# Optimization experiments

Hardware: AMD Instinct MI355X
Metric: run time of the kernel (lower is better)

The kernel has to match this reference:

```python
import jax, jax.numpy as jnp
import numpy as np

SEQ_LEN = 4096
D_IN = 2048
D_OUT = 2048
DROPOUT_P = 0.5


def setup_inputs() -> dict:
    key = jax.random.key(0)
    kx, kq, kk, kv = jax.random.split(key, 4)
    return {
        "x": jax.random.normal(kx, (SEQ_LEN, D_IN), dtype=jnp.float32),
        "W_query": jax.random.uniform(kq, (D_IN, D_OUT), dtype=jnp.float32),
        "W_key": jax.random.uniform(kk, (D_IN, D_OUT), dtype=jnp.float32),
        "W_value": jax.random.uniform(kv, (D_IN, D_OUT), dtype=jnp.float32),
    }


def reference(x, W_query, W_key, W_value):
    # projections: [S, d_in] @ [d_in, d_out] -> [S, d_out]
    queries = x @ W_query
    keys = x @ W_key
    values = x @ W_value
    # full score matrix [S, S]
    attn_scores = queries @ keys.T
    S = attn_scores.shape[0]
    causal_mask = jnp.triu(jnp.ones((S, S), dtype=bool), k=1)
    masked = jnp.where(causal_mask, -jnp.inf, attn_scores)
    scale = jnp.sqrt(jnp.asarray(keys.shape[-1], dtype=masked.dtype))
    attn_weights = jax.nn.softmax(masked / scale, axis=1)
    # dropout p=0.5 (train mode), inverted scaling, deterministic key
    keep = jax.random.bernoulli(jax.random.key(42), 1.0 - DROPOUT_P, attn_weights.shape)
    attn_weights = jnp.where(keep, attn_weights / (1.0 - DROPOUT_P), 0.0)
    context_vec = attn_weights @ values  # [S, d_out]
    return context_vec
```

## Files before the change

### kernel.cpp

```cpp
#include <hip/hip_runtime.h>
#include <cstdint>
#include <cstddef>
#include <cmath>

#define SEQ 4096
#define DM  2048

typedef unsigned int u32;
typedef unsigned short u16;
typedef __attribute__((ext_vector_type(8))) short bf16x8;
typedef __attribute__((ext_vector_type(4))) float f32x4;
typedef __attribute__((ext_vector_type(16))) float f32x16;

__device__ __forceinline__ u16 f2bf(float f) {
  u32 u = __float_as_uint(f);
  return (u16)((u + 0x7FFFu + ((u >> 16) & 1u)) >> 16);
}
__device__ __forceinline__ float bf2f(u16 h) { return __uint_as_float(((u32)h) << 16); }

__device__ __forceinline__ size_t s_base(int row) {
  const int b = row >> 7;
  return (size_t)8192 * b * (b + 1) + (size_t)128 * (row & 127) * (b + 1);
}

__device__ __forceinline__ u32 rotl32(u32 x, int r) { return (x << r) | (x >> (32 - r)); }

__device__ __forceinline__ void tf2x32(u32 c0, u32 c1, u32& o0, u32& o1) {
  const u32 k0 = 0u, k1 = 42u, k2 = 0x1BD11BDAu ^ 0u ^ 42u;
  u32 x0 = c0 + k0;
  u32 x1 = c1 + k1;
#define TFR(r) { x0 += x1; x1 = rotl32(x1, (r)); x1 ^= x0; }
  TFR(13) TFR(15) TFR(26) TFR(6)   x0 += k1; x1 += k2 + 1u;
  TFR(17) TFR(29) TFR(16) TFR(24)  x0 += k2; x1 += k0 + 2u;
  TFR(13) TFR(15) TFR(26) TFR(6)   x0 += k0; x1 += k1 + 3u;
  TFR(17) TFR(29) TFR(16) TFR(24)  x0 += k1; x1 += k2 + 4u;
  TFR(13) TFR(15) TFR(26) TFR(6)   x0 += k2; x1 += k0 + 5u;
#undef TFR
  o0 = x0; o1 = x1;
}

__device__ __forceinline__ bool dropout_keep(u32 idx) {
  u32 a, b; tf2x32(0u, idx, a, b);
  return (((a ^ b) & 0x80000000u) == 0u);
}

__device__ __forceinline__ void g2l16(const void* g, void* l) {
  __builtin_amdgcn_global_load_lds((const __attribute__((address_space(1))) u32*)g,
                                   (__attribute__((address_space(3))) u32*)l, 16, 0, 0);
}

#define MFMA16(a, b, c) __builtin_amdgcn_mfma_f32_16x16x32_bf16(a, b, c, 0, 0, 0)
#define MFMA32(a, b, c) __builtin_amdgcn_mfma_f32_32x32x16_bf16(a, b, c, 0, 0, 0)


__device__ __forceinline__ void gemm_core(
    const u16* __restrict__ Ah, const u16* __restrict__ Bh,
    int lda, int ldb, int rowBlock, int colBlock, int kmax,
    f32x4 (&acc)[4][4], u16* smem)
{
  u16* Als = smem;
  u16* Bls = smem + 8192;
  const int tid  = threadIdx.x;
  const int wid  = tid >> 6;
  const int lane = tid & 63;
  const int wr   = (wid & 1) << 6;
  const int wc   = (wid >> 1) << 6;
  const int lrow = lane & 15;
  const int lk   = (((lane >> 4) ^ ((lrow >> 1) & 3)) << 3);
  const int srow = wid * 32 + (lane >> 2);
  const int skol = (((lane & 3) ^ ((lane >> 3) & 3)) << 3);

  const f32x4 zero = {0.f, 0.f, 0.f, 0.f};
#pragma unroll
  for (int i = 0; i < 4; ++i)
#pragma unroll
    for (int j = 0; j < 4; ++j) acc[i][j] = zero;

  for (int kb = 0; kb < kmax; kb += 64) {
#pragma unroll
    for (int h = 0; h < 2; ++h)
#pragma unroll
      for (int t = 0; t < 2; ++t) {
        const size_t ga = (size_t)(rowBlock + srow + t * 16) * lda + kb + h * 32 + skol;
        const size_t gb = (size_t)(colBlock + srow + t * 16) * ldb + kb + h * 32 + skol;
        const int lo = h * 4096 + (wid * 32 + t * 16) * 32;
        g2l16(Ah + ga, &Als[lo]);
        g2l16(Bh + gb, &Bls[lo]);
      }
    __syncthreads();

#pragma unroll
    for (int h = 0; h < 2; ++h) {
      bf16x8 ah[4], bh[4];
#pragma unroll
      for (int r = 0; r < 4; ++r) {
        ah[r] = *(const bf16x8*)&Als[h * 4096 + (wr + r * 16 + lrow) * 32 + lk];
        bh[r] = *(const bf16x8*)&Bls[h * 4096 + (wc + r * 16 + lrow) * 32 + lk];
      }
#pragma unroll
      for (int r = 0; r < 4; ++r)
#pragma unroll
        for (int c = 0; c < 4; ++c)
          acc[r][c] = MFMA16(ah[r], bh[c], acc[r][c]);
    }
    __syncthreads();
  }
}

__global__ __launch_bounds__(256) void k_split_all(
    const float* __restrict__ X, u16* __restrict__ Xh, u16* __restrict__ Xl,
    const float* __restrict__ Wq, const float* __restrict__ Wk, const float* __restrict__ Wv,
    u16* __restrict__ Wqh, u16* __restrict__ Wql,
    u16* __restrict__ Wkh, u16* __restrict__ Wkl, u16* __restrict__ Wvh) {
  __shared__ float t[64][65];
  const int bid = blockIdx.x;
  const int tid = threadIdx.x;
  const int wid = tid >> 6, lane = tid & 63;

  if (bid < 4096) {
    const int kt16 = bid & 127;
    const int rt32 = (bid >> 7) * 4 + wid;
    const int row = rt32 * 32 + (lane & 31);
    const int col = kt16 * 16 + ((lane >> 5) << 3);
    const float* src = X + (size_t)row * DM + col;
    const float4 v0 = *(const float4*)src;
    const float4 v1 = *(const float4*)(src + 4);
    float v[8] = {v0.x, v0.y, v0.z, v0.w, v1.x, v1.y, v1.z, v1.w};
    u16 h[8], l[8];
#pragma unroll
    for (int j = 0; j < 8; ++j) {
      h[j] = f2bf(v[j]);
      l[j] = f2bf(v[j] - bf2f(h[j]));
    }
    u16* hp = Xh + (size_t)row * DM + col;
    *(ushort4*)hp = *(ushort4*)&h[0];
    *(ushort4*)(hp + 4) = *(ushort4*)&h[4];
    u16* lp = Xl + (((size_t)rt32 * 128 + kt16) * 64 + lane) * 8;
    *(ushort4*)lp = *(ushort4*)&l[0];
    *(ushort4*)(lp + 4) = *(ushort4*)&l[4];
    return;
  }

  const int r = bid - 4096;
  const int z = r >> 10;
  const int rem = r & 1023;
  const int n0 = (rem & 31) * 64, k0 = (rem >> 5) * 64;
  const float* W = (z == 0) ? Wq : (z == 1) ? Wk : Wv;
  u16* Oh = (z == 0) ? Wqh : (z == 1) ? Wkh : Wvh;
  u16* Ol = (z == 0) ? Wql : Wkl;
  const int tx = tid & 63, ty = tid >> 6;
#pragma unroll
  for (int i = 0; i < 16; ++i)
    t[ty * 16 + i][tx] = W[(size_t)(k0 + ty * 16 + i) * DM + n0 + tx];
  __syncthreads();
  {
    const int nl = tid >> 2, kc = (tid & 3) * 16;
    u16 h[16];
#pragma unroll
    for (int i = 0; i < 16; ++i) h[i] = f2bf(t[kc + i][nl]);
    u16* hp = Oh + (size_t)(n0 + nl) * DM + k0 + kc;
#pragma unroll
    for (int i = 0; i < 4; ++i) *(ushort4*)(hp + i * 4) = *(ushort4*)&h[i * 4];
  }
  if (z < 2) {
#pragma unroll
    for (int tt = 0; tt < 2; ++tt) {
      const int idx = wid * 2 + tt;
      const int rt = idx >> 2, kt = idx & 3;
      const int nl = rt * 32 + (lane & 31);
      const int kc = kt * 16 + ((lane >> 5) << 3);
      u16 l[8];
#pragma unroll
      for (int j = 0; j < 8; ++j) {
        const float v = t[kc + j][nl];
        l[j] = f2bf(v - bf2f(f2bf(v)));
      }
      const int rtg = (n0 >> 5) + rt, ktg = (k0 >> 4) + kt;
      u16* lp = Ol + (((size_t)rtg * (DM / 16) + ktg) * 64 + lane) * 8;
      *(ushort4*)lp = *(ushort4*)&l[0];
      *(ushort4*)(lp + 4) = *(ushort4*)&l[4];
    }
  }
}

__global__ __launch_bounds__(512, 2) void k_proj_qk(
    const u16* __restrict__ Xh, const u16* __restrict__ Xl,
    const u16* __restrict__ Wqh, const u16* __restrict__ Wql,
    const u16* __restrict__ Wkh, const u16* __restrict__ Wkl,
    u16* __restrict__ Qh, u16* __restrict__ Ql,
    u16* __restrict__ Kh, u16* __restrict__ Kl, float rscaleQ)
{
  __shared__ __align__(16) u16 smem[65536];
  const int z = blockIdx.z;
  const u16* __restrict__ Bw = z ? Wkh : Wqh;
  const u16* __restrict__ Bl = z ? Wkl : Wql;
  u16* __restrict__ Oh = z ? Kh : Qh;
  u16* __restrict__ Ol = z ? Kl : Ql;
  const float rs = z ? 1.0f : rscaleQ;

  const int rowBlock = blockIdx.y * 256;
  const int colBlock = blockIdx.x * 256;
  const int tid  = threadIdx.x;
  const int wid  = tid >> 6, lane = tid & 63;
  const int wm   = wid >> 2, wn = wid & 3;
  const int l31  = lane & 31, lh = lane >> 5;
  const int srow = tid >> 2, schunk = tid & 3;
  const int sko  = ((schunk ^ ((srow >> 1) & 3)) << 3);
  const int rkey = (l31 >> 1) & 3;
  const int rtA0 = (rowBlock >> 5) + wm * 4;
  const int rtB0 = (colBlock >> 5) + wn * 2;

  f32x16 acc[4][2];
  {
    const f32x16 z16 = {0.f,0.f,0.f,0.f,0.f,0.f,0.f,0.f,0.f,0.f,0.f,0.f,0.f,0.f,0.f,0.f};
#pragma unroll
    for (int r = 0; r < 4; ++r)
#pragma unroll
      for (int c = 0; c < 2; ++c) acc[r][c] = z16;
  }
  bf16x8 alo0[4], blo0[2], alo1[4], blo1[2];

#define QK_STG(hh, pp) { \
    g2l16(Xh + (size_t)(rowBlock + (pp)*128 + srow) * DM + kbn + (hh)*32 + sko, \
          &smem[bufN + (hh)*8192 + (pp)*4096 + tid*8]); \
    g2l16(Bw + (size_t)(colBlock + (pp)*128 + srow) * DM + kbn + (hh)*32 + sko, \
          &smem[bufN + 16384 + (hh)*8192 + (pp)*4096 + tid*8]); }

#define QK_LO(AV, BV, kt) { \
    const int kk_ = (kt); \
    _Pragma("unroll") for (int r_ = 0; r_ < 4; ++r_) \
      AV[r_] = *(const bf16x8*)(Xl + (((size_t)(rtA0 + r_) * 128 + kk_) * 64 + lane) * 8); \
    _Pragma("unroll") for (int c_ = 0; c_ < 2; ++c_) \
      BV[c_] = *(const bf16x8*)(Bl + (((size_t)(rtB0 + c_) * 128 + kk_) * 64 + lane) * 8); }

#define QK_PH(qq, ALC, BLC, ALN, BLN, STMT, ktn) { \
    __builtin_amdgcn_sched_barrier(0); \
    QK_LO(ALN, BLN, ktn); \
    __builtin_amdgcn_sched_barrier(0); \
    STMT; \
    bf16x8 ah[4], bh[2]; \
    const int cl_ = ((qq) & 1) * 2 + lh; \
    const int hx_ = (qq) >> 1; \
    _Pragma("unroll") for (int r_ = 0; r_ < 4; ++r_) \
      ah[r_] = *(const bf16x8*)&smem[bufC + ((hx_*256 + wm*128 + r_*32 + l31) << 5) + ((cl_ ^ rkey) << 3)]; \
    _Pragma("unroll") for (int c_ = 0; c_ < 2; ++c_) \
      bh[c_] = *(const bf16x8*)&smem[bufC + 16384 + ((hx_*256 + wn*64 + c_*32 + l31) << 5) + ((cl_ ^ rkey) << 3)]; \
    __builtin_amdgcn_s_setprio(1); \
    _Pragma("unroll") for (int r_ = 0; r_ < 4; ++r_) \
      _Pragma("unroll") for (int c_ = 0; c_ < 2; ++c_) { \
        acc[r_][c_] = MFMA32(ah[r_], bh[c_], acc[r_][c_]); \
        acc[r_][c_] = MFMA32(ah[r_], BLC[c_], acc[r_][c_]); \
        acc[r_][c_] = MFMA32(ALC[r_], bh[c_], acc[r_][c_]); } \
    __builtin_amdgcn_s_setprio(0); }

  {
    const size_t kbn = 0; const int bufN = 0;
    QK_STG(0,0) QK_STG(0,1) QK_STG(1,0) QK_STG(1,1)
  }
  QK_LO(alo0, blo0, 0);
  asm volatile("s_waitcnt vmcnt(0)" ::: "memory");
  __builtin_amdgcn_s_barrier();

  for (int t = 0; t < 32; ++t) {
    const int bufC = (t & 1) << 15;
    const int bufN = bufC ^ 32768;
    const size_t kbn = (size_t)(t + 1) * 64;
    const bool more = (t < 31);
    const int g4 = t * 4;
    QK_PH(0, alo0, blo0, alo1, blo1, if (more) { QK_STG(0,0) QK_STG(0,1) }, g4 + 1)
    QK_PH(1, alo1, blo1, alo0, blo0, if (more) { QK_STG(1,0) QK_STG(1,1) }, g4 + 2)
    QK_PH(2, alo0, blo0, alo1, blo1, ;, g4 + 3)
    QK_PH(3, alo1, blo1, alo0, blo0, ;, (g4 + 4 < 128 ? g4 + 4 : 127))
    asm volatile("s_waitcnt vmcnt(0)" ::: "memory");
    __builtin_amdgcn_s_barrier();
  }
#undef QK_PH
#undef QK_LO
#undef QK_STG

  __syncthreads();
  u16* scr = smem + wid * 8192;
  const int r0g = rowBlock + wm * 128;
  const int c0g = colBlock + wn * 64;
#pragma unroll
  for (int r = 0; r < 4; ++r)
#pragma unroll
    for (int c = 0; c < 2; ++c) {
      const int colL = c * 32 + l31;
#pragma unroll
      for (int g = 0; g < 4; ++g)
#pragma unroll
        for (int e = 0; e < 4; ++e) {
          const int rowL = r * 32 + 8 * g + 4 * lh + e;
          const float v = acc[r][c][g * 4 + e] * rs;
          const u16 h = f2bf(v);
          Oh[(size_t)(r0g + rowL) * DM + c0g + colL] = h;
          scr[rowL * 64 + (((colL >> 3) ^ (rowL & 7)) << 3) + (colL & 7)] =
              f2bf(v - bf2f(h));
        }
    }
  asm volatile("s_waitcnt lgkmcnt(0)" ::: "memory");
  __builtin_amdgcn_sched_barrier(0);
#pragma unroll
  for (int rt = 0; rt < 4; ++rt)
#pragma unroll
    for (int kt = 0; kt < 4; ++kt) {
      const int rowL = rt * 32 + l31;
      const int cl2 = kt * 2 + lh;
      const bf16x8 v = *(const bf16x8*)&scr[rowL * 64 + ((cl2 ^ (rowL & 7)) << 3)];
      const int rtg = (rowBlock >> 5) + wm * 4 + rt;
      const int ktg = (colBlock >> 4) + wn * 4 + kt;
      *(bf16x8*)(Ol + (((size_t)rtg * 128 + ktg) * 64 + lane) * 8) = v;
    }
}

__device__ __forceinline__ void scores_body(
    const u16* __restrict__ Qh, const u16* __restrict__ Ql,
    const u16* __restrict__ Kh, const u16* __restrict__ Kl,
    float* __restrict__ S, u16* smem)
{
  const int bid = blockIdx.x;
  int by = (int)((sqrtf(4.0f * (float)bid + 1.0f) - 1.0f) * 0.5f);
  while ((by + 1) * (by + 2) <= bid) ++by;
  while (by * (by + 1) > bid) --by;
  const int bx = bid - by * (by + 1);
  const int rowBlock = by * 256, colBlock = bx * 128;

  const int tid  = threadIdx.x;
  const int wid  = tid >> 6, lane = tid & 63;
  const int wm   = wid >> 1, wn = wid & 1;
  const int l31  = lane & 31, lh = lane >> 5;
  const int srow = tid >> 2, schunk = tid & 3;
  const int sko  = ((schunk ^ ((srow >> 1) & 3)) << 3);
  const int rkey = (l31 >> 1) & 3;

  f32x16 acc[2][2];
  {
    const f32x16 z16 = {0.f,0.f,0.f,0.f,0.f,0.f,0.f,0.f,0.f,0.f,0.f,0.f,0.f,0.f,0.f,0.f};
#pragma unroll
    for (int r = 0; r < 2; ++r)
#pragma unroll
      for (int c = 0; c < 2; ++c) acc[r][c] = z16;
  }

#define S_STG_AHI(pp) g2l16(Qh + (size_t)(rowBlock + (pp)*128 + srow) * DM + kbn + sko, \
                            &smem[bufN + (pp)*4096 + tid*8]);
#define S_STG_BHI     g2l16(Kh + (size_t)(colBlock + srow) * DM + kbn + sko, \
                            &smem[bufN + 8192 + tid*8]);
#define S_STG_ALO(ss) { const int idx_ = (ss)*8 + wid; \
    g2l16(Ql + ((size_t)((rowBlock >> 5) + (idx_ >> 1)) * 128 + (kbn >> 4) + (idx_ & 1)) * 512 + lane*8, \
          &smem[bufN + 12288 + idx_*512 + lane*8]); }
#define S_STG_BLO     { const int idx_ = wid; \
    g2l16(Kl + ((size_t)((colBlock >> 5) + (idx_ >> 1)) * 128 + (kbn >> 4) + (idx_ & 1)) * 512 + lane*8, \
          &smem[bufN + 20480 + idx_*512 + lane*8]); }

#define S_PHASE(qq) { \
    bf16x8 ah[2], bh[2], al[2], bl[2]; \
    const int cl_ = (qq)*2 + lh; \
    _Pragma("unroll") for (int r_ = 0; r_ < 2; ++r_) \
      ah[r_] = *(const bf16x8*)&smem[bufC + ((wm*64 + r_*32 + l31) << 5) + ((cl_ ^ rkey) << 3)]; \
    _Pragma("unroll") for (int c_ = 0; c_ < 2; ++c_) \
      bh[c_] = *(const bf16x8*)&smem[bufC + 8192 + ((wn*64 + c_*32 + l31) << 5) + ((cl_ ^ rkey) << 3)]; \
    _Pragma("unroll") for (int r_ = 0; r_ < 2; ++r_) \
      al[r_] = *(const bf16x8*)&smem[bufC + 12288 + ((wm*2 + r_)*2 + (qq))*512 + lane*8]; \
    _Pragma("unroll") for (int c_ = 0; c_ < 2; ++c_) \
      bl[c_] = *(const bf16x8*)&smem[bufC + 20480 + ((wn*2 + c_)*2 + (qq))*512 + lane*8]; \
    __builtin_amdgcn_s_setprio(1); \
    _Pragma("unroll") for (int r_ = 0; r_ < 2; ++r_) \
      _Pragma("unroll") for (int c_ = 0; c_ < 2; ++c_) { \
        acc[r_][c_] = MFMA32(ah[r_], bh[c_], acc[r_][c_]); \
        acc[r_][c_] = MFMA32(ah[r_], bl[c_], acc[r_][c_]); \
        acc[r_][c_] = MFMA32(al[r_], bh[c_], acc[r_][c_]); } \
    __builtin_amdgcn_s_setprio(0); }

  {
    const size_t kbn = 0; const int bufN = 0;
    S_STG_AHI(0) S_STG_AHI(1) S_STG_BHI
    S_STG_ALO(0) S_STG_ALO(1) S_STG_BLO
  }
  asm volatile("s_waitcnt vmcnt(0)" ::: "memory");
  __builtin_amdgcn_s_barrier();

  for (int t = 0; t < 64; ++t) {
    const int bufC = (t & 1) * 24576;
    const int bufN = bufC ^ 24576;
    const size_t kbn = (size_t)(t + 1) * 32;
    if (t < 63) { S_STG_AHI(0) S_STG_AHI(1) S_STG_BHI }
    __builtin_amdgcn_sched_barrier(0);
    S_PHASE(0)
    if (t < 63) { S_STG_ALO(0) S_STG_ALO(1) S_STG_BLO }
    __builtin_amdgcn_sched_barrier(0);
    S_PHASE(1)
    asm volatile("s_waitcnt vmcnt(0)" ::: "memory");
    __builtin_amdgcn_s_barrier();
  }
#undef S_PHASE
#undef S_STG_BLO
#undef S_STG_ALO
#undef S_STG_BHI
#undef S_STG_AHI

  const int r0 = rowBlock + wm * 64, c0 = colBlock + wn * 64;
#pragma unroll
  for (int r = 0; r < 2; ++r)
#pragma unroll
    for (int c = 0; c < 2; ++c) {
      const int col = c0 + c * 32 + l31;
#pragma unroll
      for (int g = 0; g < 4; ++g)
#pragma unroll
        for (int e = 0; e < 4; ++e) {
          const int row = r0 + r * 32 + 8 * g + 4 * lh + e;
          if ((col >> 7) <= (row >> 7))
            S[s_base(row) + col] = acc[r][c][g * 4 + e];
        }
    }
}

__device__ __forceinline__ void projv_body(
    const u16* __restrict__ Xh, const u16* __restrict__ Wvh,
    u16* __restrict__ Vt, int vbid, u16* smem)
{
  const int rowBlock = (vbid >> 4) * 256;
  const int colBlock = (vbid & 15) * 128;
  const int tid  = threadIdx.x;
  const int wid  = tid >> 6, lane = tid & 63;
  const int wm   = wid >> 1, wn = wid & 1;
  const int l31  = lane & 31, lh = lane >> 5;
  const int srow = tid >> 2, schunk = tid & 3;
  const int sko  = ((schunk ^ ((srow >> 1) & 3)) << 3);
  const int rkey = (l31 >> 1) & 3;

  f32x16 acc[2][2];
  {
    const f32x16 z16 = {0.f,0.f,0.f,0.f,0.f,0.f,0.f,0.f,0.f,0.f,0.f,0.f,0.f,0.f,0.f,0.f};
#pragma unroll
    for (int r = 0; r < 2; ++r)
#pragma unroll
      for (int c = 0; c < 2; ++c) acc[r][c] = z16;
  }

#define V_STGA(hh, pp) g2l16(Xh + (size_t)(rowBlock + (pp)*128 + srow) * DM + kbn + (hh)*32 + sko, \
                             &smem[bufN + (hh)*8192 + (pp)*4096 + tid*8]);
#define V_STGB(hh)     g2l16(Wvh + (size_t)(colBlock + srow) * DM + kbn + (hh)*32 + sko, \
                             &smem[bufN + 16384 + (hh)*4096 + tid*8]);

#define V_PH(qq, STMT) { \
    __builtin_amdgcn_sched_barrier(0); \
    STMT; \
    bf16x8 ah[2], bh[2]; \
    const int cl_ = ((qq) & 1) * 2 + lh; \
    const int hx_ = (qq) >> 1; \
    _Pragma("unroll") for (int r_ = 0; r_ < 2; ++r_) \
      ah[r_] = *(const bf16x8*)&smem[bufC + ((hx_*256 + wm*64 + r_*32 + l31) << 5) + ((cl_ ^ rkey) << 3)]; \
    _Pragma("unroll") for (int c_ = 0; c_ < 2; ++c_) \
      bh[c_] = *(const bf16x8*)&smem[bufC + 16384 + ((hx_*128 + wn*64 + c_*32 + l31) << 5) + ((cl_ ^ rkey) << 3)]; \
    __builtin_amdgcn_s_setprio(1); \
    _Pragma("unroll") for (int r_ = 0; r_ < 2; ++r_) \
      _Pragma("unroll") for (int c_ = 0; c_ < 2; ++c_) \
        acc[r_][c_] = MFMA32(ah[r_], bh[c_], acc[r_][c_]); \
    __builtin_amdgcn_s_setprio(0); }

  {
    const size_t kbn = 0; const int bufN = 0;
    V_STGA(0,0) V_STGA(0,1) V_STGA(1,0) V_STGA(1,1) V_STGB(0) V_STGB(1)
  }
  asm volatile("s_waitcnt vmcnt(0)" ::: "memory");
  __builtin_amdgcn_s_barrier();

  for (int t = 0; t < 32; ++t) {
    const int bufC = (t & 1) * 24576;
    const int bufN = bufC ^ 24576;
    const size_t kbn = (size_t)(t + 1) * 64;
    const bool more = (t < 31);
    V_PH(0, if (more) { V_STGA(0,0) V_STGA(0,1) V_STGB(0) })
    V_PH(1, if (more) { V_STGA(1,0) V_STGA(1,1) V_STGB(1) })
    V_PH(2, ;)
    V_PH(3, ;)
    asm volatile("s_waitcnt vmcnt(0)" ::: "memory");
    __builtin_amdgcn_s_barrier();
  }
#undef V_PH
#undef V_STGB
#undef V_STGA

  const int vr0 = rowBlock + wm * 64;
#pragma unroll
  for (int r = 0; r < 2; ++r)
#pragma unroll
    for (int c = 0; c < 2; ++c) {
      const int col = colBlock + wn * 64 + c * 32 + l31;
#pragma unroll
      for (int g = 0; g < 4; ++g) {
        ushort4 pk;
        pk.x = f2bf(acc[r][c][g * 4 + 0]);
        pk.y = f2bf(acc[r][c][g * 4 + 1]);
        pk.z = f2bf(acc[r][c][g * 4 + 2]);
        pk.w = f2bf(acc[r][c][g * 4 + 3]);
        *(ushort4*)(Vt + (size_t)col * SEQ + vr0 + r * 32 + 8 * g + 4 * lh) = pk;
      }
    }
}

__global__ __launch_bounds__(512, 2) void k_scores_v(
    const u16* __restrict__ Qh, const u16* __restrict__ Ql,
    const u16* __restrict__ Kh, const u16* __restrict__ Kl,
    float* __restrict__ S,
    const u16* __restrict__ Xh, const u16* __restrict__ Wvh,
    u16* __restrict__ Vt)
{
  __shared__ __align__(16) u16 smem[49152];
  if (blockIdx.x < 272) {
    scores_body(Qh, Ql, Kh, Kl, S, smem);
  } else {
    projv_body(Xh, Wvh, Vt, blockIdx.x - 272, smem);
  }
}

__global__ __launch_bounds__(256) void k_softmax_dropout(const float* __restrict__ S,
                                                         u16* __restrict__ P) {
  const int row = blockIdx.x;
  const int n = row + 1;
  const int nt = (n + 1023) >> 10;
  const int tid = threadIdx.x;
  __shared__ float buf[SEQ];
  __shared__ float red[4];
  __shared__ float bcast;
  const float* srow = S + s_base(row);

  float lmax = -INFINITY;
  for (int t = 0; t < nt; ++t) {
    int j4 = tid + t * 256;
    float4 v = *(const float4*)(srow + (size_t)j4 * 4);
    int b = j4 * 4;
    float x0 = (b + 0 < n) ? v.x : -INFINITY;
    float x1 = (b + 1 < n) ? v.y : -INFINITY;
    float x2 = (b + 2 < n) ? v.z : -INFINITY;
    float x3 = (b + 3 < n) ? v.w : -INFINITY;
    buf[b + 0] = x0; buf[b + 1] = x1; buf[b + 2] = x2; buf[b + 3] = x3;
    lmax = fmaxf(lmax, fmaxf(fmaxf(x0, x1), fmaxf(x2, x3)));
  }
  for (int off = 32; off > 0; off >>= 1) lmax = fmaxf(lmax, __shfl_down(lmax, off, 64));
  if ((tid & 63) == 0) red[tid >> 6] = lmax;
  __syncthreads();
  if (tid == 0) bcast = fmaxf(fmaxf(red[0], red[1]), fmaxf(red[2], red[3]));
  __syncthreads();
  const float m = bcast;

  float lsum = 0.f;
  for (int t = 0; t < nt; ++t) {
    int b = (tid + t * 256) * 4;
    float e0 = expf(buf[b + 0] - m);
    float e1 = expf(buf[b + 1] - m);
    float e2 = expf(buf[b + 2] - m);
    float e3 = expf(buf[b + 3] - m);
    buf[b + 0] = e0; buf[b + 1] = e1; buf[b + 2] = e2; buf[b + 3] = e3;
    lsum += (e0 + e1) + (e2 + e3);
  }
  for (int off = 32; off > 0; off >>= 1) lsum += __shfl_down(lsum, off, 64);
  if ((tid & 63) == 0) red[tid >> 6] = lsum;
  __syncthreads();
  if (tid == 0) bcast = (red[0] + red[1]) + (red[2] + red[3]);
  __syncthreads();
  const float total = bcast;

  u16* prow = P + (size_t)row * SEQ;
  const int zeroEnd = ((row >> 7) + 1) << 7;
  for (int j = tid; j < zeroEnd; j += 256) {
    float out = 0.f;
    if (j < n) {
      const float w = buf[j] / total;
      out = dropout_keep((u32)(row * SEQ + j)) ? w * 2.0f : 0.f;
    }
    prow[j] = f2bf(out);
  }
}

__global__ __launch_bounds__(256) void k_pv(const u16* __restrict__ P,
                                            const u16* __restrict__ Vt,
                                            float* __restrict__ O) {
  __shared__ __align__(16) u16 smem[16384];
  const int by = (SEQ / 128 - 1) - blockIdx.y;
  f32x4 acc[4][4];
  gemm_core(P, Vt, SEQ, SEQ, by * 128, blockIdx.x * 128, (by + 1) * 128, acc, smem);

  const int lane = threadIdx.x & 63, wid = threadIdx.x >> 6;
  const int r0 = by * 128 + ((wid & 1) << 6) + ((lane >> 4) << 2);
  const int c0 = blockIdx.x * 128 + ((wid >> 1) << 6) + (lane & 15);
#pragma unroll
  for (int r = 0; r < 4; ++r)
#pragma unroll
    for (int c = 0; c < 4; ++c)
#pragma unroll
      for (int e = 0; e < 4; ++e)
        O[(size_t)(r0 + r * 16 + e) * DM + (c0 + c * 16)] = acc[r][c][e];
}

extern "C" void kernel_launch(void* const* d_in, const int* in_sizes, int n_in,
                              void* d_out, int out_size, void* d_ws, size_t ws_size,
                              hipStream_t stream) {
  const float* x  = (const float*)d_in[0];
  const float* Wq = (const float*)d_in[1];
  const float* Wk = (const float*)d_in[2];
  const float* Wv = (const float*)d_in[3];

  const size_t PL = (size_t)SEQ * DM;
  const size_t WL = (size_t)DM * DM;
  u16* base = (u16*)d_ws;
  u16* Qh = base;
  u16* Ql = Qh + PL;
  u16* Kh = Ql + PL;
  u16* Kl = Kh + PL;
  u16* Vt = Kl + PL;
  u16* P  = base;
  u16* regA = Vt + PL;
  u16* Xh  = regA;
  u16* Xl  = Xh + PL;
  u16* Wqh = Xl + PL;
  u16* Wql = Wqh + WL;
  u16* Wkh = Wql + WL;
  u16* Wkl = Wkh + WL;
  u16* Wvh = Wkl + WL;
  float* S = (float*)Xl;

  const float rscale = 1.0f / sqrtf(2048.0f);
  k_split_all<<<dim3(4096 + 3 * 1024), dim3(256), 0, stream>>>(
      x, Xh, Xl, Wq, Wk, Wv, Wqh, Wql, Wkh, Wkl, Wvh);
  k_proj_qk<<<dim3(DM / 256, SEQ / 256, 2), dim3(512), 0, stream>>>(
      Xh, Xl, Wqh, Wql, Wkh, Wkl, Qh, Ql, Kh, Kl, rscale);
  k_scores_v<<<dim3(272 + 256), dim3(512), 0, stream>>>(
      Qh, Ql, Kh, Kl, S, Xh, Wvh, Vt);
  k_softmax_dropout<<<dim3(SEQ), dim3(256), 0, stream>>>(S, P);
  k_pv<<<dim3(DM / 128, SEQ / 128), dim3(256), 0, stream>>>(P, Vt, (float*)d_out);
}
```

Measured before the change: 583.5 us.

## Rewrite P·V GEMM with 256-row tiles, double-buffered LDS and 32x32 MFMA

```diff
diff --git a/kernel.cpp b/kernel.cpp
--- a/kernel.cpp
+++ b/kernel.cpp
@@ -52,60 +52,6 @@
 #define MFMA16(a, b, c) __builtin_amdgcn_mfma_f32_16x16x32_bf16(a, b, c, 0, 0, 0)
 #define MFMA32(a, b, c) __builtin_amdgcn_mfma_f32_32x32x16_bf16(a, b, c, 0, 0, 0)
 
-
-__device__ __forceinline__ void gemm_core(
-    const u16* __restrict__ Ah, const u16* __restrict__ Bh,
-    int lda, int ldb, int rowBlock, int colBlock, int kmax,
-    f32x4 (&acc)[4][4], u16* smem)
-{
-  u16* Als = smem;
-  u16* Bls = smem + 8192;
-  const int tid  = threadIdx.x;
-  const int wid  = tid >> 6;
-  const int lane = tid & 63;
-  const int wr   = (wid & 1) << 6;
-  const int wc   = (wid >> 1) << 6;
-  const int lrow = lane & 15;
-  const int lk   = (((lane >> 4) ^ ((lrow >> 1) & 3)) << 3);
-  const int srow = wid * 32 + (lane >> 2);
-  const int skol = (((lane & 3) ^ ((lane >> 3) & 3)) << 3);
-
-  const f32x4 zero = {0.f, 0.f, 0.f, 0.f};
-#pragma unroll
-  for (int i = 0; i < 4; ++i)
-#pragma unroll
-    for (int j = 0; j < 4; ++j) acc[i][j] = zero;
-
-  for (int kb = 0; kb < kmax; kb += 64) {
-#pragma unroll
-    for (int h = 0; h < 2; ++h)
-#pragma unroll
-      for (int t = 0; t < 2; ++t) {
-        const size_t ga = (size_t)(rowBlock + srow + t * 16) * lda + kb + h * 32 + skol;
-        const size_t gb = (size_t)(colBlock + srow + t * 16) * ldb + kb + h * 32 + skol;
-        const int lo = h * 4096 + (wid * 32 + t * 16) * 32;
-        g2l16(Ah + ga, &Als[lo]);
-        g2l16(Bh + gb, &Bls[lo]);
-      }
-    __syncthreads();
-
-#pragma unroll
-    for (int h = 0; h < 2; ++h) {
-      bf16x8 ah[4], bh[4];
-#pragma unroll
-      for (int r = 0; r < 4; ++r) {
-        ah[r] = *(const bf16x8*)&Als[h * 4096 + (wr + r * 16 + lrow) * 32 + lk];
-        bh[r] = *(const bf16x8*)&Bls[h * 4096 + (wc + r * 16 + lrow) * 32 + lk];
-      }
-#pragma unroll
-      for (int r = 0; r < 4; ++r)
-#pragma unroll
-        for (int c = 0; c < 4; ++c)
-          acc[r][c] = MFMA16(ah[r], bh[c], acc[r][c]);
-    }
-    __syncthreads();
-  }
-}
 
 __global__ __launch_bounds__(256) void k_split_all(
     const float* __restrict__ X, u16* __restrict__ Xh, u16* __restrict__ Xl,
@@ -565,7 +511,7 @@
   const float total = bcast;
 
   u16* prow = P + (size_t)row * SEQ;
-  const int zeroEnd = ((row >> 7) + 1) << 7;
+  const int zeroEnd = ((row >> 8) + 1) << 8;
   for (int j = tid; j < zeroEnd; j += 256) {
     float out = 0.f;
     if (j < n) {
@@ -576,24 +522,91 @@
   }
 }
 
-__global__ __launch_bounds__(256) void k_pv(const u16* __restrict__ P,
-                                            const u16* __restrict__ Vt,
-                                            float* __restrict__ O) {
-  __shared__ __align__(16) u16 smem[16384];
-  const int by = (SEQ / 128 - 1) - blockIdx.y;
-  f32x4 acc[4][4];
-  gemm_core(P, Vt, SEQ, SEQ, by * 128, blockIdx.x * 128, (by + 1) * 128, acc, smem);
-
-  const int lane = threadIdx.x & 63, wid = threadIdx.x >> 6;
-  const int r0 = by * 128 + ((wid & 1) << 6) + ((lane >> 4) << 2);
-  const int c0 = blockIdx.x * 128 + ((wid >> 1) << 6) + (lane & 15);
-#pragma unroll
-  for (int r = 0; r < 4; ++r)
-#pragma unroll
-    for (int c = 0; c < 4; ++c)
-#pragma unroll
-      for (int e = 0; e < 4; ++e)
-        O[(size_t)(r0 + r * 16 + e) * DM + (c0 + c * 16)] = acc[r][c][e];
+__global__ __launch_bounds__(512, 2) void k_pv(const u16* __restrict__ P,
+                                               const u16* __restrict__ Vt,
+                                               float* __restrict__ O) {
+  __shared__ __align__(16) u16 smem[49152];
+  const int by = (SEQ / 256 - 1) - blockIdx.y;
+  const int rowBlock = by * 256;
+  const int colBlock = blockIdx.x * 128;
+  const int kmax = rowBlock + 256;
+  const int nt = kmax >> 6;
+  const int tid  = threadIdx.x;
+  const int wid  = tid >> 6, lane = tid & 63;
+  const int wm   = wid >> 1, wn = wid & 1;
+  const int l31  = lane & 31, lh = lane >> 5;
+  const int srow = tid >> 2, schunk = tid & 3;
+  const int sko  = ((schunk ^ ((srow >> 1) & 3)) << 3);
+  const int rkey = (l31 >> 1) & 3;
+
+  f32x16 acc[2][2];
+  {
+    const f32x16 z16 = {0.f,0.f,0.f,0.f,0.f,0.f,0.f,0.f,0.f,0.f,0.f,0.f,0.f,0.f,0.f,0.f};
+#pragma unroll
+    for (int r = 0; r < 2; ++r)
+#pragma unroll
+      for (int c = 0; c < 2; ++c) acc[r][c] = z16;
+  }
+
+#define PV_STGA(hh, pp) g2l16(P + (size_t)(rowBlock + (pp)*128 + srow) * SEQ + kbn + (hh)*32 + sko, \
+                              &smem[bufN + (hh)*8192 + (pp)*4096 + tid*8]);
+#define PV_STGB(hh)     g2l16(Vt + (size_t)(colBlock + srow) * SEQ + kbn + (hh)*32 + sko, \
+                              &smem[bufN + 16384 + (hh)*4096 + tid*8]);
+
+#define PV_PH(qq, STMT) { \
+    __builtin_amdgcn_sched_barrier(0); \
+    STMT; \
+    bf16x8 ah[2], bh[2]; \
+    const int cl_ = ((qq) & 1) * 2 + lh; \
+    const int hx_ = (qq) >> 1; \
+    _Pragma("unroll") for (int r_ = 0; r_ < 2; ++r_) \
+      ah[r_] = *(const bf16x8*)&smem[bufC + ((hx_*256 + wm*64 + r_*32 + l31) << 5) + ((cl_ ^ rkey) << 3)]; \
+    _Pragma("unroll") for (int c_ = 0; c_ < 2; ++c_) \
+      bh[c_] = *(const bf16x8*)&smem[bufC + 16384 + ((hx_*128 + wn*64 + c_*32 + l31) << 5) + ((cl_ ^ rkey) << 3)]; \
+    __builtin_amdgcn_s_setprio(1); \
+    _Pragma("unroll") for (int r_ = 0; r_ < 2; ++r_) \
+      _Pragma("unroll") for (int c_ = 0; c_ < 2; ++c_) \
+        acc[r_][c_] = MFMA32(ah[r_], bh[c_], acc[r_][c_]); \
+    __builtin_amdgcn_s_setprio(0); }
+
+  {
+    const size_t kbn = 0; const int bufN = 0;
+    PV_STGA(0,0) PV_STGA(0,1) PV_STGA(1,0) PV_STGA(1,1) PV_STGB(0) PV_STGB(1)
+  }
+  asm volatile("s_waitcnt vmcnt(0)" ::: "memory");
+  __builtin_amdgcn_s_barrier();
+
+  for (int t = 0; t < nt; ++t) {
+    const int bufC = (t & 1) * 24576;
+    const int bufN = bufC ^ 24576;
+    const size_t kbn = (size_t)(t + 1) * 64;
+    const bool more = (t < nt - 1);
+    PV_PH(0, if (more) { PV_STGA(0,0) PV_STGA(0,1) PV_STGB(0) })
+    PV_PH(1, if (more) { PV_STGA(1,0) PV_STGA(1,1) PV_STGB(1) })
+    PV_PH(2, ;)
+    PV_PH(3, ;)
+    asm volatile("s_waitcnt vmcnt(0)" ::: "memory");
+    __builtin_amdgcn_s_barrier();
+  }
+#undef PV_PH
+#undef PV_STGB
+#undef PV_STGA
+
+  const int r0 = rowBlock + wm * 64;
+  const int c0 = colBlock + wn * 64;
+#pragma unroll
+  for (int r = 0; r < 2; ++r)
+#pragma unroll
+    for (int c = 0; c < 2; ++c) {
+      const int col = c0 + c * 32 + l31;
+#pragma unroll
+      for (int g = 0; g < 4; ++g)
+#pragma unroll
+        for (int e = 0; e < 4; ++e) {
+          const int row = r0 + r * 32 + 8 * g + 4 * lh + e;
+          O[(size_t)row * DM + col] = acc[r][c][g * 4 + e];
+        }
+    }
 }
 
 extern "C" void kernel_launch(void* const* d_in, const int* in_sizes, int n_in,
@@ -631,5 +644,5 @@
   k_scores_v<<<dim3(272 + 256), dim3(512), 0, stream>>>(
       Qh, Ql, Kh, Kl, S, Xh, Wvh, Vt);
   k_softmax_dropout<<<dim3(SEQ), dim3(256), 0, stream>>>(S, P);
-  k_pv<<<dim3(DM / 128, SEQ / 128), dim3(256), 0, stream>>>(P, Vt, (float*)d_out);
-}
+  k_pv<<<dim3(DM / 128, SEQ / 256), dim3(512), 0, stream>>>(P, Vt, (float*)d_out);
+}
```

Result: slower. 614.9 us (+5.4%).
